# Performance work log

Hardware: AMD Instinct MI355X
Metric: run time of the kernel (lower is better)

Reference implementation:

```python
import jax, jax.numpy as jnp
import numpy as np

B, S, D = 4, 1024, 2048
H = 4096
NE = 8
TOPK = 2


def setup_inputs() -> dict:
    key = jax.random.key(0)
    ks = jax.random.split(key, 9)
    s = lambda fan_in: 1.0 / np.sqrt(fan_in)
    return {
        "x": jax.random.normal(ks[0], (B, S, D), dtype=jnp.float32),
        "W1": jax.random.normal(ks[1], (NE, D, H), dtype=jnp.float32) * s(D),
        "b1": jnp.zeros((NE, H), dtype=jnp.float32),
        "W2": jax.random.normal(ks[2], (NE, H, H), dtype=jnp.float32) * s(H),
        "b2": jnp.zeros((NE, H), dtype=jnp.float32),
        "W3": jax.random.normal(ks[3], (NE, H, D), dtype=jnp.float32) * s(H),
        "b3": jnp.zeros((NE, D), dtype=jnp.float32),
        "Wg": jax.random.normal(ks[4], (D, NE), dtype=jnp.float32) * s(D),
        "bg": jnp.zeros((NE,), dtype=jnp.float32),
    }


def reference(x, W1, b1, W2, b2, W3, b3, Wg, bg):
    # Gating: softmax over experts, then top-k
    gate_logits = jnp.einsum("bsd,dn->bsn", x, Wg) + bg          # [B,S,NE]
    gate_weights = jax.nn.softmax(gate_logits, axis=-1)
    topv, topi = jax.lax.top_k(gate_weights, TOPK)               # [B,S,K]

    # Dense compute of ALL experts (faithful to original)
    h = jax.nn.gelu(jnp.einsum("bsd,ndh->nbsh", x, W1) + b1[:, None, None, :], approximate=False)
    h = jax.nn.gelu(jnp.einsum("nbsh,nhf->nbsf", h, W2) + b2[:, None, None, :], approximate=False)
    eo = jnp.einsum("nbsf,nfd->nbsd", h, W3) + b3[:, None, None, :]  # [NE,B,S,D]

    # Weighted combine of top-k experts per token via sparse one-hot weights
    comb = jnp.sum(jax.nn.one_hot(topi, NE, dtype=x.dtype) * topv[..., None], axis=-2)  # [B,S,NE]
    out = jnp.einsum("nbsd,bsn->bsd", eo, comb)
    return out
```

## Files before the change

### kernel.cpp

```cpp
#include <hip/hip_runtime.h>
#include <math.h>

#define NT 4096
#define Dm 2048
#define Hm 4096
#define NEx 8
#define CAPROWS 9216

typedef float f32x4 __attribute__((ext_vector_type(4)));
typedef _Float16 f16x8 __attribute__((ext_vector_type(8)));

__global__ void k_init(int* meta) {
    if (threadIdx.x < NEx) meta[threadIdx.x] = 0;
}

__device__ __forceinline__ void conv_tile(const float* __restrict__ src, _Float16* __restrict__ dst,
                                          int K, int N, int t, float (*tile)[65]) {
    int nx = N >> 6, nk = K >> 6;
    int nb = t % nx;
    int kb = (t / nx) % nk;
    int e  = t / (nx * nk);
    int n0 = nb * 64, k0 = kb * 64;
    size_t ebase = (size_t)e * (size_t)K * (size_t)N;
    const float* S = src + ebase;
    _Float16* Dd = dst + ebase;
    int tx = threadIdx.x & 15, ty = threadIdx.x >> 4;
#pragma unroll
    for (int p = 0; p < 4; ++p) {
        int kr = p * 16 + ty;
        f32x4 v = __builtin_nontemporal_load((const f32x4*)(S + (size_t)(k0 + kr) * N + n0 + tx * 4));
        tile[kr][tx * 4 + 0] = v[0]; tile[kr][tx * 4 + 1] = v[1];
        tile[kr][tx * 4 + 2] = v[2]; tile[kr][tx * 4 + 3] = v[3];
    }
    __syncthreads();
    int n = threadIdx.x >> 2, seg = threadIdx.x & 3;
    f16x8 o0, o1;
#pragma unroll
    for (int j = 0; j < 8; ++j) o0[j] = (_Float16)tile[seg * 16 + j][n];
#pragma unroll
    for (int j = 0; j < 8; ++j) o1[j] = (_Float16)tile[seg * 16 + 8 + j][n];
    _Float16* dp = Dd + (size_t)(n0 + n) * K + k0 + seg * 16;
    __builtin_nontemporal_store(o0, (f16x8*)dp);
    __builtin_nontemporal_store(o1, (f16x8*)(dp + 8));
}

__global__ __launch_bounds__(256, 2) void k_convw(const float* __restrict__ src,
                                                  _Float16* __restrict__ dst, int K, int N) {
    __shared__ float tile[64][65];
    conv_tile(src, dst, K, N, blockIdx.x, tile);
}

__global__ __launch_bounds__(256, 2)
void k_gateconv(const float* __restrict__ x, const float* __restrict__ Wg,
                const float* __restrict__ bg, int* __restrict__ meta,
                int* __restrict__ list, float* __restrict__ topw,
                const float* __restrict__ csrc, _Float16* __restrict__ cdst,
                int cK, int cN) {
    __shared__ float tile[64][65];
    const int bid = blockIdx.x;
    if (bid >= NT / 4) {
        conv_tile(csrc, cdst, cK, cN, bid - NT / 4, tile);
        return;
    }
    int lane = threadIdx.x & 63;
    int t = bid * 4 + (threadIdx.x >> 6);
    const float* xr = x + (size_t)t * Dm;
    double acc[NEx];
#pragma unroll
    for (int j = 0; j < NEx; ++j) acc[j] = 0.0;
    for (int d = lane; d < Dm; d += 64) {
        double xv = (double)xr[d];
        const float* wr = Wg + (size_t)d * NEx;
#pragma unroll
        for (int j = 0; j < NEx; ++j) acc[j] += xv * (double)wr[j];
    }
#pragma unroll
    for (int off = 32; off > 0; off >>= 1) {
#pragma unroll
        for (int j = 0; j < NEx; ++j) acc[j] += __shfl_xor(acc[j], off, 64);
    }
    if (lane == 0) {
        double l[NEx];
#pragma unroll
        for (int j = 0; j < NEx; ++j) l[j] = acc[j] + (double)bg[j];
        double m = l[0];
        for (int j = 1; j < NEx; ++j) m = l[j] > m ? l[j] : m;
        double s = 0.0, ev[NEx];
        for (int j = 0; j < NEx; ++j) { ev[j] = exp(l[j] - m); s += ev[j]; }
        int i0 = 0; double v0 = l[0];
        for (int j = 1; j < NEx; ++j) if (l[j] > v0) { v0 = l[j]; i0 = j; }
        int i1 = -1; double v1 = -1e300;
        for (int j = 0; j < NEx; ++j) if (j != i0 && l[j] > v1) { v1 = l[j]; i1 = j; }
        topw[2 * t]     = (float)(ev[i0] / s);
        topw[2 * t + 1] = (float)(ev[i1] / s);
        int p0 = atomicAdd(&meta[i0], 1); list[i0 * NT + p0] = 2 * t;
        int p1 = atomicAdd(&meta[i1], 1); list[i1 * NT + p1] = 2 * t + 1;
    }
}

__global__ void k_plan(int* meta) {
    if (threadIdx.x == 0 && blockIdx.x == 0) {
        int tot = 0;
        for (int e = 0; e < NEx; ++e) {
            int c = meta[e];
            meta[8 + e] = c;
            int cp = (c + 127) & ~127;
            meta[16 + e] = cp;
            meta[24 + e] = tot;
            tot += cp;
        }
        meta[32] = tot;
    }
}

__global__ void k_gather(const float* __restrict__ x, const int* __restrict__ meta,
                         const int* __restrict__ list, int* __restrict__ pos_of,
                         _Float16* __restrict__ Xg) {
    int r = blockIdx.x;
    if (r >= meta[32]) return;
    int e = 0;
    while (r >= meta[24 + e + 1]) ++e;
    int i = r - meta[24 + e];
    _Float16* dst = Xg + (size_t)r * Dm + threadIdx.x * 8;
    if (i < meta[8 + e]) {
        int v = list[e * NT + i];
        int t = v >> 1;
        if (threadIdx.x == 0) pos_of[v] = r;
        const float* src = x + (size_t)t * Dm + threadIdx.x * 8;
        f32x4 a = *(const f32x4*)(src);
        f32x4 b = *(const f32x4*)(src + 4);
        f16x8 o;
        o[0] = (_Float16)a[0]; o[1] = (_Float16)a[1]; o[2] = (_Float16)a[2]; o[3] = (_Float16)a[3];
        o[4] = (_Float16)b[0]; o[5] = (_Float16)b[1]; o[6] = (_Float16)b[2]; o[7] = (_Float16)b[3];
        *(f16x8*)dst = o;
    } else {
        f16x8 z = (f16x8)(_Float16)0.0f;
        *(f16x8*)dst = z;
    }
}

__device__ __forceinline__ void gload16(const void* g, void* l) {
    __builtin_amdgcn_global_load_lds((__attribute__((address_space(1))) void*)(g),
                                     (__attribute__((address_space(3))) void*)(l),
                                     16, 0, 0);
}

__device__ __forceinline__ float gelu_f(float v) {
    return 0.5f * v * (1.0f + erff(v * 0.70710678118654752f));
}

template <int KDIM, int NDIM, bool GELU>
__global__ __launch_bounds__(256, 4)
void k_gemmconv(const _Float16* __restrict__ Abase, const _Float16* __restrict__ Wt,
                const float* __restrict__ bias, void* __restrict__ Cout,
                const int* __restrict__ meta,
                const float* __restrict__ c1src, _Float16* __restrict__ c1dst, int c1K, int c1N, int n1,
                const float* __restrict__ c2src, _Float16* __restrict__ c2dst, int c2K, int c2N,
                int nGemm) {
    __shared__ char smem[32768];
    const int bid = blockIdx.x;
    if (bid >= nGemm) {
        const int t = bid - nGemm;
        if (t < n1) conv_tile(c1src, c1dst, c1K, c1N, t, (float(*)[65])smem);
        else        conv_tile(c2src, c2dst, c2K, c2N, t - n1, (float(*)[65])smem);
        return;
    }

    constexpr int GX = NDIM / 128;
    constexpr int GY = 32;
    constexpr int NBLK = GX * GY;
    const int e = bid / NBLK;
    const int f = bid % NBLK;
    const int fp = (f & 7) * (NBLK >> 3) + (f >> 3);
    const int nt = fp / GY;
    const int mt = fp % GY;
    const int cp = meta[16 + e];
    if (mt * 128 >= cp) return;
    const int row0 = meta[24 + e] + mt * 128;

    _Float16* ldsA = (_Float16*)smem;
    _Float16* ldsB = (_Float16*)(smem + 16384);

    const int tid = threadIdx.x;
    const int lane = tid & 63;
    const int wv = tid >> 6;
    const int wm = wv >> 1, wn = wv & 1;

    const char* Ag = (const char*)(Abase + (size_t)row0 * KDIM);
    const char* Bg = (const char*)(Wt + ((size_t)e * NDIM + (size_t)nt * 128) * KDIM);

    int soff[4];
#pragma unroll
    for (int r = 0; r < 4; ++r) {
        int L = r * 4096 + tid * 16;
        int row = L >> 7;
        int col = L & 127;
        int scol = col ^ ((row & 7) << 4);
        soff[r] = row * (KDIM * 2) + scol;
    }

    f32x4 acc[4][4];
#pragma unroll
    for (int i = 0; i < 4; ++i)
#pragma unroll
        for (int j = 0; j < 4; ++j)
            acc[i][j] = (f32x4){0.f, 0.f, 0.f, 0.f};

    int abase[4], aswz[4], bbase[4], bswz[4];
#pragma unroll
    for (int m = 0; m < 4; ++m) {
        int rA = wm * 64 + m * 16 + (lane & 15);
        abase[m] = rA * 128;
        aswz[m] = (rA & 7) << 4;
    }
#pragma unroll
    for (int n = 0; n < 4; ++n) {
        int rB = wn * 64 + n * 16 + (lane & 15);
        bbase[n] = rB * 128;
        bswz[n] = (rB & 7) << 4;
    }
    const int hib = (lane >> 4) * 16;

    const char* cldsA = (const char*)ldsA;
    const char* cldsB = (const char*)ldsB;

    for (int kt = 0; kt < KDIM / 64; ++kt) {
        const int kbyte = kt * 128;
#pragma unroll
        for (int r = 0; r < 4; ++r) {
            gload16(Ag + (soff[r] + kbyte), (char*)ldsA + r * 4096 + tid * 16);
            gload16(Bg + (soff[r] + kbyte), (char*)ldsB + r * 4096 + tid * 16);
        }
        __syncthreads();
#pragma unroll
        for (int ks = 0; ks < 2; ++ks) {
            const int cbs = ks * 64 + hib;
            f16x8 av[4], bv[4];
#pragma unroll
            for (int m = 0; m < 4; ++m)
                av[m] = *(const f16x8*)(cldsA + abase[m] + (cbs ^ aswz[m]));
#pragma unroll
            for (int n = 0; n < 4; ++n)
                bv[n] = *(const f16x8*)(cldsB + bbase[n] + (cbs ^ bswz[n]));
#pragma unroll
            for (int m = 0; m < 4; ++m)
#pragma unroll
                for (int n = 0; n < 4; ++n)
                    acc[m][n] = __builtin_amdgcn_mfma_f32_16x16x32_f16(av[m], bv[n], acc[m][n], 0, 0, 0);
        }
        __syncthreads();
    }

    const int lcol = lane & 15;
    const int rowq = (lane >> 4) * 4;
#pragma unroll
    for (int m = 0; m < 4; ++m) {
#pragma unroll
        for (int n = 0; n < 4; ++n) {
            const int gcol = nt * 128 + wn * 64 + n * 16 + lcol;
            const float bb = bias[(size_t)e * NDIM + gcol];
#pragma unroll
            for (int v = 0; v < 4; ++v) {
                const int grow = row0 + wm * 64 + m * 16 + rowq + v;
                float val = acc[m][n][v] + bb;
                if constexpr (GELU) {
                    ((_Float16*)Cout)[(size_t)grow * NDIM + gcol] = (_Float16)gelu_f(val);
                } else {
                    ((float*)Cout)[(size_t)grow * NDIM + gcol] = val;
                }
            }
        }
    }
}

__global__ void k_combine(const float* __restrict__ eo, const int* __restrict__ pos_of,
                          const float* __restrict__ topw, float* __restrict__ out) {
    int t = blockIdx.x;
    int r0 = pos_of[2 * t], r1 = pos_of[2 * t + 1];
    float w0 = topw[2 * t], w1 = topw[2 * t + 1];
    const f32x4* e0 = (const f32x4*)(eo + (size_t)r0 * Dm);
    const f32x4* e1 = (const f32x4*)(eo + (size_t)r1 * Dm);
    f32x4* op = (f32x4*)(out + (size_t)t * Dm);
    for (int i = threadIdx.x; i < Dm / 4; i += 256) {
        f32x4 a = e0[i], b = e1[i];
        op[i] = a * w0 + b * w1;
    }
}

extern "C" void kernel_launch(void* const* d_in, const int* in_sizes, int n_in,
                              void* d_out, int out_size, void* d_ws, size_t ws_size,
                              hipStream_t stream) {
    const float* x  = (const float*)d_in[0];
    const float* W1 = (const float*)d_in[1];
    const float* b1 = (const float*)d_in[2];
    const float* W2 = (const float*)d_in[3];
    const float* b2 = (const float*)d_in[4];
    const float* W3 = (const float*)d_in[5];
    const float* b3 = (const float*)d_in[6];
    const float* Wg = (const float*)d_in[7];
    const float* bg = (const float*)d_in[8];
    float* out = (float*)d_out;
    (void)in_sizes; (void)n_in; (void)out_size;

    char* ws = (char*)d_ws;
    int*   meta   = (int*)ws;
    int*   list   = (int*)(ws + 256);
    int*   pos_of = (int*)(ws + 256 + 131072);
    float* topw   = (float*)(ws + 256 + 131072 + 32768);
    size_t off = 196864;

    const int nC1 = (Hm / 64) * (Dm / 64) * NEx;
    const int nC2 = (Hm / 64) * (Hm / 64) * NEx;
    const int nC3 = (Dm / 64) * (Hm / 64) * NEx;
    const int nG12 = NEx * (Hm / 128) * 32;
    const int nG3  = NEx * (Dm / 128) * 32;

    const size_t sXg  = (size_t)CAPROWS * Dm * 2;
    const size_t sWb1 = (size_t)NEx * Dm * Hm * 2;
    const size_t sWb2 = (size_t)NEx * Hm * Hm * 2;
    const size_t sWb3 = (size_t)NEx * Hm * Dm * 2;
    const size_t sH   = (size_t)CAPROWS * Hm * 2;

    const size_t needPar = off + sXg + sWb1 + sWb2 + sWb3 + sH + sH;

    if (ws_size >= needPar) {
        _Float16* Xg  = (_Float16*)(ws + off); off += sXg;
        _Float16* Wb1 = (_Float16*)(ws + off); off += sWb1;
        _Float16* Wb2 = (_Float16*)(ws + off); off += sWb2;
        _Float16* Wb3 = (_Float16*)(ws + off); off += sWb3;
        _Float16* h1  = (_Float16*)(ws + off); off += sH;
        _Float16* h2  = (_Float16*)(ws + off); off += sH;
        float*    eo  = (float*)Wb1;

        k_init<<<1, 64, 0, stream>>>(meta);
        k_gateconv<<<NT / 4 + nC1, 256, 0, stream>>>(x, Wg, bg, meta, list, topw,
                                                     W1, Wb1, Dm, Hm);
        k_plan<<<1, 1, 0, stream>>>(meta);
        k_gather<<<CAPROWS, 256, 0, stream>>>(x, meta, list, pos_of, Xg);

        k_gemmconv<Dm, Hm, true><<<nG12 + nC2 + nC3, 256, 0, stream>>>(
            Xg, Wb1, b1, (void*)h1, meta,
            W2, Wb2, Hm, Hm, nC2,
            W3, Wb3, Hm, Dm,
            nG12);
        k_gemmconv<Hm, Hm, true><<<nG12, 256, 0, stream>>>(
            h1, Wb2, b2, (void*)h2, meta,
            (const float*)0, (_Float16*)0, 0, 0, 0,
            (const float*)0, (_Float16*)0, 0, 0,
            nG12);
        k_gemmconv<Hm, Dm, false><<<nG3, 256, 0, stream>>>(
            h2, Wb3, b3, (void*)eo, meta,
            (const float*)0, (_Float16*)0, 0, 0, 0,
            (const float*)0, (_Float16*)0, 0, 0,
            nG3);

        k_combine<<<NT, 256, 0, stream>>>(eo, pos_of, topw, out);
    } else {
        _Float16* Xg = (_Float16*)(ws + off); off += sXg;
        _Float16* Wb = (_Float16*)(ws + off); off += sWb2;
        _Float16* h2 = (_Float16*)(ws + off); off += sH;
        _Float16* h1 = (_Float16*)(ws + off);
        float*    eo = (float*)(ws + off);

        k_init<<<1, 64, 0, stream>>>(meta);
        k_gateconv<<<NT / 4, 256, 0, stream>>>(x, Wg, bg, meta, list, topw,
                                               (const float*)0, (_Float16*)0, 0, 0);
        k_plan<<<1, 1, 0, stream>>>(meta);
        k_gather<<<CAPROWS, 256, 0, stream>>>(x, meta, list, pos_of, Xg);

        k_convw<<<nC1, 256, 0, stream>>>(W1, Wb, Dm, Hm);
        k_gemmconv<Dm, Hm, true><<<nG12, 256, 0, stream>>>(
            Xg, Wb, b1, (void*)h1, meta,
            (const float*)0, (_Float16*)0, 0, 0, 0,
            (const float*)0, (_Float16*)0, 0, 0, nG12);

        k_convw<<<nC2, 256, 0, stream>>>(W2, Wb, Hm, Hm);
        k_gemmconv<Hm, Hm, true><<<nG12, 256, 0, stream>>>(
            h1, Wb, b2, (void*)h2, meta,
            (const float*)0, (_Float16*)0, 0, 0, 0,
            (const float*)0, (_Float16*)0, 0, 0, nG12);

        k_convw<<<nC3, 256, 0, stream>>>(W3, Wb, Hm, Dm);
        k_gemmconv<Hm, Dm, false><<<nG3, 256, 0, stream>>>(
            h2, Wb, b3, (void*)eo, meta,
            (const float*)0, (_Float16*)0, 0, 0, 0,
            (const float*)0, (_Float16*)0, 0, 0, nG3);

        k_combine<<<NT, 256, 0, stream>>>(eo, pos_of, topw, out);
    }
}
```

Before: 1.121 ms.

## Redistribute weight-conversion tiles across gate, gather and GEMM kernels

The fp32-to-fp16 weight conversion tiles are spread more evenly across the launch sequence. Part of W2's conversion moves into the gating kernel and part into the gather kernel. The rest of W2 runs beside the first GEMM, and W3's conversion moves beside the second GEMM. The aim is to balance the memory-bound conversion work against the compute-bound GEMMs so that no single launch carries a long conversion tail. The risk is extra contention in kernels that used to be light, and a fixed split that may not match each phase's length.

```diff
diff --git a/kernel.cpp b/kernel.cpp
--- a/kernel.cpp
+++ b/kernel.cpp
@@ -54,12 +54,14 @@
 void k_gateconv(const float* __restrict__ x, const float* __restrict__ Wg,
                 const float* __restrict__ bg, int* __restrict__ meta,
                 int* __restrict__ list, float* __restrict__ topw,
-                const float* __restrict__ csrc, _Float16* __restrict__ cdst,
-                int cK, int cN) {
+                const float* __restrict__ c1src, _Float16* __restrict__ c1dst, int c1K, int c1N, int n1,
+                const float* __restrict__ c2src, _Float16* __restrict__ c2dst, int c2K, int c2N) {
     __shared__ float tile[64][65];
     const int bid = blockIdx.x;
     if (bid >= NT / 4) {
-        conv_tile(csrc, cdst, cK, cN, bid - NT / 4, tile);
+        const int t = bid - NT / 4;
+        if (t < n1) conv_tile(c1src, c1dst, c1K, c1N, t, tile);
+        else        conv_tile(c2src, c2dst, c2K, c2N, t - n1, tile);
         return;
     }
     int lane = threadIdx.x & 63;
@@ -115,8 +117,15 @@
 
 __global__ void k_gather(const float* __restrict__ x, const int* __restrict__ meta,
                          const int* __restrict__ list, int* __restrict__ pos_of,
-                         _Float16* __restrict__ Xg) {
+                         _Float16* __restrict__ Xg,
+                         const float* __restrict__ csrc, _Float16* __restrict__ cdst,
+                         int cK, int cN, int cBase) {
     int r = blockIdx.x;
+    if (r >= CAPROWS) {
+        __shared__ float tile[64][65];
+        conv_tile(csrc, cdst, cK, cN, cBase + (r - CAPROWS), tile);
+        return;
+    }
     if (r >= meta[32]) return;
     int e = 0;
     while (r >= meta[24 + e + 1]) ++e;
@@ -154,15 +163,13 @@
 void k_gemmconv(const _Float16* __restrict__ Abase, const _Float16* __restrict__ Wt,
                 const float* __restrict__ bias, void* __restrict__ Cout,
                 const int* __restrict__ meta,
-                const float* __restrict__ c1src, _Float16* __restrict__ c1dst, int c1K, int c1N, int n1,
-                const float* __restrict__ c2src, _Float16* __restrict__ c2dst, int c2K, int c2N,
+                const float* __restrict__ csrc, _Float16* __restrict__ cdst,
+                int cK, int cN, int cBase,
                 int nGemm) {
     __shared__ char smem[32768];
     const int bid = blockIdx.x;
     if (bid >= nGemm) {
-        const int t = bid - nGemm;
-        if (t < n1) conv_tile(c1src, c1dst, c1K, c1N, t, (float(*)[65])smem);
-        else        conv_tile(c2src, c2dst, c2K, c2N, t - n1, (float(*)[65])smem);
+        conv_tile(csrc, cdst, cK, cN, cBase + (bid - nGemm), (float(*)[65])smem);
         return;
     }
 
@@ -312,6 +319,9 @@
     const int nC1 = (Hm / 64) * (Dm / 64) * NEx;
     const int nC2 = (Hm / 64) * (Hm / 64) * NEx;
     const int nC3 = (Dm / 64) * (Hm / 64) * NEx;
+    const int C2A = 12288;
+    const int C2B = 8192;
+    const int C2C = nC2 - C2A - C2B;
     const int nG12 = NEx * (Hm / 128) * 32;
     const int nG3  = NEx * (Dm / 128) * 32;
 
@@ -333,25 +343,26 @@
         float*    eo  = (float*)Wb1;
 
         k_init<<<1, 64, 0, stream>>>(meta);
-        k_gateconv<<<NT / 4 + nC1, 256, 0, stream>>>(x, Wg, bg, meta, list, topw,
-                                                     W1, Wb1, Dm, Hm);
+        k_gateconv<<<NT / 4 + nC1 + C2A, 256, 0, stream>>>(
+            x, Wg, bg, meta, list, topw,
+            W1, Wb1, Dm, Hm, nC1,
+            W2, Wb2, Hm, Hm);
         k_plan<<<1, 1, 0, stream>>>(meta);
-        k_gather<<<CAPROWS, 256, 0, stream>>>(x, meta, list, pos_of, Xg);
-
-        k_gemmconv<Dm, Hm, true><<<nG12 + nC2 + nC3, 256, 0, stream>>>(
+        k_gather<<<CAPROWS + C2B, 256, 0, stream>>>(
+            x, meta, list, pos_of, Xg,
+            W2, Wb2, Hm, Hm, C2A);
+
+        k_gemmconv<Dm, Hm, true><<<nG12 + C2C, 256, 0, stream>>>(
             Xg, Wb1, b1, (void*)h1, meta,
-            W2, Wb2, Hm, Hm, nC2,
-            W3, Wb3, Hm, Dm,
+            W2, Wb2, Hm, Hm, C2A + C2B,
             nG12);
-        k_gemmconv<Hm, Hm, true><<<nG12, 256, 0, stream>>>(
+        k_gemmconv<Hm, Hm, true><<<nG12 + nC3, 256, 0, stream>>>(
             h1, Wb2, b2, (void*)h2, meta,
-            (const float*)0, (_Float16*)0, 0, 0, 0,
-            (const float*)0, (_Float16*)0, 0, 0,
+            W3, Wb3, Hm, Dm, 0,
             nG12);
         k_gemmconv<Hm, Dm, false><<<nG3, 256, 0, stream>>>(
             h2, Wb3, b3, (void*)eo, meta,
             (const float*)0, (_Float16*)0, 0, 0, 0,
-            (const float*)0, (_Float16*)0, 0, 0,
             nG3);
 
         k_combine<<<NT, 256, 0, stream>>>(eo, pos_of, topw, out);
@@ -363,28 +374,29 @@
         float*    eo = (float*)(ws + off);
 
         k_init<<<1, 64, 0, stream>>>(meta);
-        k_gateconv<<<NT / 4, 256, 0, stream>>>(x, Wg, bg, meta, list, topw,
-                                               (const float*)0, (_Float16*)0, 0, 0);
+        k_gateconv<<<NT / 4, 256, 0, stream>>>(
+            x, Wg, bg, meta, list, topw,
+            (const float*)0, (_Float16*)0, 0, 0, 0,
+            (const float*)0, (_Float16*)0, 0, 0);
         k_plan<<<1, 1, 0, stream>>>(meta);
-        k_gather<<<CAPROWS, 256, 0, stream>>>(x, meta, list, pos_of, Xg);
+        k_gather<<<CAPROWS, 256, 0, stream>>>(
+            x, meta, list, pos_of, Xg,
+            (const float*)0, (_Float16*)0, 0, 0, 0);
 
         k_convw<<<nC1, 256, 0, stream>>>(W1, Wb, Dm, Hm);
         k_gemmconv<Dm, Hm, true><<<nG12, 256, 0, stream>>>(
             Xg, Wb, b1, (void*)h1, meta,
-            (const float*)0, (_Float16*)0, 0, 0, 0,
-            (const float*)0, (_Float16*)0, 0, 0, nG12);
+            (const float*)0, (_Float16*)0, 0, 0, 0, nG12);
 
         k_convw<<<nC2, 256, 0, stream>>>(W2, Wb, Hm, Hm);
         k_gemmconv<Hm, Hm, true><<<nG12, 256, 0, stream>>>(
             h1, Wb, b2, (void*)h2, meta,
-            (const float*)0, (_Float16*)0, 0, 0, 0,
-            (const float*)0, (_Float16*)0, 0, 0, nG12);
+            (const float*)0, (_Float16*)0, 0, 0, 0, nG12);
 
         k_convw<<<nC3, 256, 0, stream>>>(W3, Wb, Hm, Dm);
         k_gemmconv<Hm, Dm, false><<<nG3, 256, 0, stream>>>(
             h2, Wb, b3, (void*)eo, meta,
-            (const float*)0, (_Float16*)0, 0, 0, 0,
-            (const float*)0, (_Float16*)0, 0, 0, nG3);
+            (const float*)0, (_Float16*)0, 0, 0, 0, nG3);
 
         k_combine<<<NT, 256, 0, stream>>>(eo, pos_of, topw, out);
     }
```

Result: faster. 1.093 ms (-2.4%).
